# Kernel tuning notes

Hardware: AMD Instinct MI355X
Metric: run time of the kernel (lower is better)

Reference implementation:

```python
import jax, jax.numpy as jnp
import numpy as np

NEG_SLOPE = 0.2
EPS = 1e-16


def gat_layer(x, edge_index, edge_attr, W, We, a_src, a_dst, a_edge, bias,
              add_self_loops):
    """PyG GATConv with concat=True.
    x: [N, F_in], edge_index: [2, E] (row 0 = src j, row 1 = dst i),
    edge_attr: [E, De], W: [F_in, H*C], We: [De, H*C],
    a_src/a_dst/a_edge: [H, C], bias: [H*C].
    """
    N = x.shape[0]
    H, C = a_src.shape
    if add_self_loops:
        # fill_value='mean': self-loop edge_attr = mean of incoming edge_attr per node
        dst0 = edge_index[1]
        s = jax.ops.segment_sum(edge_attr, dst0, num_segments=N)
        cnt = jax.ops.segment_sum(jnp.ones((edge_attr.shape[0], 1), edge_attr.dtype),
                                  dst0, num_segments=N)
        loop_attr = s / jnp.maximum(cnt, 1.0)
        loop_idx = jnp.arange(N, dtype=edge_index.dtype)
        edge_index = jnp.concatenate(
            [edge_index, jnp.stack([loop_idx, loop_idx])], axis=1)
        edge_attr = jnp.concatenate([edge_attr, loop_attr], axis=0)

    src, dst = edge_index[0], edge_index[1]
    h = (x @ W).reshape(N, H, C)                       # [N, H, C]
    e = (edge_attr @ We).reshape(-1, H, C)             # [E, H, C]

    alpha_src = jnp.einsum('nhc,hc->nh', h, a_src)     # [N, H]
    alpha_dst = jnp.einsum('nhc,hc->nh', h, a_dst)     # [N, H]
    alpha_edge = jnp.einsum('ehc,hc->eh', e, a_edge)   # [E, H]

    alpha = alpha_src[src] + alpha_dst[dst] + alpha_edge
    alpha = jax.nn.leaky_relu(alpha, NEG_SLOPE)

    # segment softmax over destination node
    amax = jax.ops.segment_max(alpha, dst, num_segments=N)      # [N, H]
    ex = jnp.exp(alpha - amax[dst])
    denom = jax.ops.segment_sum(ex, dst, num_segments=N)        # [N, H]
    attn = ex / (denom[dst] + EPS)                               # [E, H]

    msg = h[src] * attn[:, :, None]                              # [E, H, C]
    out = jax.ops.segment_sum(msg, dst, num_segments=N)          # [N, H, C]
    return out.reshape(N, H * C) + bias


def setup_inputs() -> dict:
    key = jax.random.key(0)
    ks = jax.random.split(key, 16)
    N, E, F_in, C, H, De = 10000, 160000, 128, 64, 8, 1
    d1 = H * C  # 512

    def glorot(k, shape):
        fan = shape[0] + shape[-1]
        s = jnp.sqrt(6.0 / fan)
        return jax.random.uniform(k, shape, jnp.float32, -s, s)

    return {
        'x': jax.random.normal(ks[0], (N, F_in), jnp.float32),
        'edge_index': jax.random.randint(ks[1], (2, E), 0, N, jnp.int32),
        'edge_attr': jax.random.normal(ks[2], (E, De), jnp.float32),
        # layer 1 params
        'W1': glorot(ks[3], (F_in, d1)),
        'We1': glorot(ks[4], (De, d1)),
        'as1': glorot(ks[5], (H, C)),
        'ad1': glorot(ks[6], (H, C)),
        'ae1': glorot(ks[7], (H, C)),
        'b1': jnp.zeros((d1,), jnp.float32),
        # layer 2 params
        'W2': glorot(ks[8], (d1, d1)),
        'We2': glorot(ks[9], (De, d1)),
        'as2': glorot(ks[10], (H, C)),
        'ad2': glorot(ks[11], (H, C)),
        'ae2': glorot(ks[12], (H, C)),
        'b2': jnp.zeros((d1,), jnp.float32),
    }


def reference(x, edge_index, edge_attr,
              W1, We1, as1, ad1, ae1, b1,
              W2, We2, as2, ad2, ae2, b2):
    h = gat_layer(x, edge_index, edge_attr, W1, We1, as1, ad1, ae1, b1,
                  add_self_loops=False)
    h = jax.nn.relu(h)
    h = gat_layer(h, edge_index, edge_attr, W2, We2, as2, ad2, ae2, b2,
                  add_self_loops=True)
    return jnp.mean(h, axis=0)  # [512]
```

## Files before the change

### kernel.cpp

```cpp
#include <hip/hip_runtime.h>
#include <hip/hip_bf16.h>

#define HD __device__ __forceinline__
typedef unsigned short u16;
typedef __attribute__((ext_vector_type(8))) short bf16x8;
typedef __attribute__((ext_vector_type(4))) float f32x4;

HD u16 f2b(float f){
  unsigned u = __float_as_uint(f);
  unsigned r = (u + 0x7fffu + ((u>>16)&1u)) >> 16;
  return (u16)r;
}
HD float b2f(short s){ return __uint_as_float(((unsigned)(u16)s)<<16); }

__global__ void k_count(const int* __restrict__ dst, const float* __restrict__ ea,
                        int* cnt, float* easum, int E){
  int e = blockIdx.x*blockDim.x + threadIdx.x;
  if (e>=E) return;
  int d = dst[e];
  atomicAdd(&cnt[d],1);
  atomicAdd(&easum[d], ea[e]);
}

__global__ __launch_bounds__(1024) void k_scan(const int* __restrict__ cnt, int* offs, int N){
  __shared__ int lds[1024];
  const int chunk = (N + 1023)/1024;
  const int b = threadIdx.x*chunk;
  int s = 0;
  for (int i=0;i<chunk;++i){ int idx=b+i; if (idx<N) s += cnt[idx]; }
  lds[threadIdx.x] = s;
  __syncthreads();
  #pragma unroll
  for (int off=1; off<1024; off<<=1){
    int t = (threadIdx.x>=(unsigned)off)? lds[threadIdx.x-off] : 0;
    __syncthreads();
    lds[threadIdx.x] += t;
    __syncthreads();
  }
  int excl = lds[threadIdx.x] - s;
  for (int i=0;i<chunk;++i){
    int idx=b+i;
    if (idx<N){ offs[idx] = excl; excl += cnt[idx]; }
  }
  if (threadIdx.x==1023) offs[N] = lds[1023];
}

__global__ void k_scatter(const int* __restrict__ src, const int* __restrict__ dst,
                          const float* __restrict__ ea, const int* __restrict__ offs,
                          int* fill, int* srcs, float* eas, int E){
  int e = blockIdx.x*blockDim.x + threadIdx.x;
  if (e>=E) return;
  int d = dst[e];
  int p = offs[d] + atomicAdd(&fill[d],1);
  srcs[p] = src[e];
  eas[p]  = ea[e];
}

__global__ void k_loopattr(const int* __restrict__ cnt, const float* __restrict__ easum,
                           float* la, int N){
  int n = blockIdx.x*blockDim.x + threadIdx.x;
  if (n>=N) return;
  la[n] = easum[n] / fmaxf((float)cnt[n], 1.f);
}

__global__ __launch_bounds__(512) void k_wedot(const float* __restrict__ We1, const float* __restrict__ ae1,
                        const float* __restrict__ We2, const float* __restrict__ ae2,
                        float* wedot){
  int which = blockIdx.x;
  const float* We = which? We2 : We1;
  const float* ae = which? ae2 : ae1;
  int hh = threadIdx.x>>6, lane = threadIdx.x&63;
  float p = We[hh*64+lane]*ae[hh*64+lane];
  #pragma unroll
  for (int o=32;o;o>>=1) p += __shfl_down(p,o);
  if (lane==0) wedot[which*8+hh] = p;
}

__global__ void k_cast_bf16(const float* __restrict__ in, u16* __restrict__ out, int total4){
  int i = (blockIdx.x*blockDim.x + threadIdx.x);
  if (i>=total4) return;
  float4 v = *(const float4*)(in + (size_t)i*4);
  ushort4 o; o.x=f2b(v.x); o.y=f2b(v.y); o.z=f2b(v.z); o.w=f2b(v.w);
  *(ushort4*)(out + (size_t)i*4) = o;
}

__global__ __launch_bounds__(256) void k_transpose_cast(const float* __restrict__ W,
                                                        u16* __restrict__ Wt, int K, int N){
  __shared__ float T[64][65];
  int k0 = blockIdx.y*64, n0 = blockIdx.x*64;
  #pragma unroll
  for (int i=0;i<16;++i){
    int id = i*256 + threadIdx.x;
    int r = id>>6, c = id&63;
    T[r][c] = W[(size_t)(k0+r)*N + n0 + c];
  }
  __syncthreads();
  #pragma unroll
  for (int i=0;i<16;++i){
    int id = i*256 + threadIdx.x;
    int rr = id>>6, cc = id&63;
    Wt[(size_t)(n0+rr)*K + k0 + cc] = f2b(T[cc][rr]);
  }
}

__global__ __launch_bounds__(256) void k_gemm_mfma(
    const u16* __restrict__ A, const u16* __restrict__ Bt,
    u16* __restrict__ Cb, int M, int N, int K){
  __shared__ char lds[(128+64)*80];
  char* As = lds;
  char* Bs = lds + 128*80;
  const int tid = threadIdx.x;
  const int lane = tid & 63, w = tid >> 6;
  const int wr = w >> 1, wc = w & 1;
  const int l15 = lane & 15, l4 = lane >> 4;
  const int m0 = blockIdx.y*128, n0 = blockIdx.x*64;

  f32x4 acc[4][2] = {};
  int aoff[4], boff[2];
  #pragma unroll
  for (int i=0;i<4;++i) aoff[i] = (wr*64 + i*16 + l15)*80 + l4*16;
  #pragma unroll
  for (int j=0;j<2;++j) boff[j] = (wc*32 + j*16 + l15)*80 + l4*16;

  for (int k0=0; k0<K; k0+=32){
    #pragma unroll
    for (int i=0;i<2;++i){
      int cid = tid*2+i;
      int r = cid>>2, c = cid&3;
      int row = m0 + r;
      float4 v = make_float4(0.f,0.f,0.f,0.f);
      if (row < M) v = *(const float4*)(A + (size_t)row*K + k0 + c*8);
      *(float4*)(As + r*80 + c*16) = v;
    }
    {
      int r = tid>>2, c = tid&3;
      float4 v = *(const float4*)(Bt + (size_t)(n0+r)*K + k0 + c*8);
      *(float4*)(Bs + r*80 + c*16) = v;
    }
    __syncthreads();
    bf16x8 a[4], b[2];
    #pragma unroll
    for (int i=0;i<4;++i) a[i] = *reinterpret_cast<const bf16x8*>(As + aoff[i]);
    #pragma unroll
    for (int j=0;j<2;++j) b[j] = *reinterpret_cast<const bf16x8*>(Bs + boff[j]);
    #pragma unroll
    for (int i=0;i<4;++i)
      #pragma unroll
      for (int j=0;j<2;++j)
        acc[i][j] = __builtin_amdgcn_mfma_f32_16x16x32_bf16(a[i], b[j], acc[i][j], 0,0,0);
    __syncthreads();
  }
  #pragma unroll
  for (int i=0;i<4;++i){
    #pragma unroll
    for (int j=0;j<2;++j){
      #pragma unroll
      for (int r=0;r<4;++r){
        int row = m0 + wr*64 + i*16 + l4*4 + r;
        int col = n0 + wc*32 + j*16 + l15;
        if (row < M) Cb[(size_t)row*N + col] = f2b(acc[i][j][r]);
      }
    }
  }
}

__global__ __launch_bounds__(256) void k_alpha_nodes(const u16* __restrict__ hb,
    const float* __restrict__ a_s, const float* __restrict__ a_d,
    float* asrc, float* adst, int N){
  int n = blockIdx.x*4 + (threadIdx.x>>6);
  if (n>=N) return;
  int lane = threadIdx.x&63;
  int c0 = lane*8;
  bf16x8 v = *(const bf16x8*)(hb + (size_t)n*512 + c0);
  float s = 0.f, d = 0.f;
  #pragma unroll
  for (int j=0;j<8;++j){
    float f = b2f(v[j]);
    s = fmaf(f, a_s[c0+j], s);
    d = fmaf(f, a_d[c0+j], d);
  }
  #pragma unroll
  for (int o=1;o<8;o<<=1){ s += __shfl_xor(s,o); d += __shfl_xor(d,o); }
  if ((lane&7)==0){ int hh = lane>>3; asrc[n*8+hh]=s; adst[n*8+hh]=d; }
}

__global__ __launch_bounds__(256) void k_softmax(
    const int* __restrict__ srcs, const float* __restrict__ eas,
    const int* __restrict__ offs,
    const float* __restrict__ asrc, const float* __restrict__ adst,
    const float* __restrict__ wedot, const float* __restrict__ la,
    float* __restrict__ exn, float* __restrict__ inv, float* __restrict__ aselfx,
    int N, int self_flag){
  int n = blockIdx.x*4 + (threadIdx.x>>6);
  if (n>=N) return;
  int lane = threadIdx.x&63;
  int hh = lane&7, esub = lane>>3;
  int beg = offs[n], end = offs[n+1];
  float wd = wedot[hh];
  float adn = adst[n*8+hh];

  float mx = -1e30f;
  for (int p0=beg; p0<end; p0+=8){
    int p = p0 + esub;
    if (p<end){
      int s = srcs[p];
      float a = asrc[s*8+hh] + adn + eas[p]*wd;
      a = a>0.f ? a : 0.2f*a;
      exn[(size_t)p*8+hh] = a;
      mx = fmaxf(mx, a);
    }
  }
  float aself = 0.f;
  if (self_flag){
    float a = asrc[n*8+hh] + adn + la[n]*wd;
    aself = a>0.f ? a : 0.2f*a;
    if (esub==0) mx = fmaxf(mx, aself);
  }
  mx = fmaxf(mx, __shfl_xor(mx, 8));
  mx = fmaxf(mx, __shfl_xor(mx, 16));
  mx = fmaxf(mx, __shfl_xor(mx, 32));

  float sum = 0.f;
  for (int p0=beg; p0<end; p0+=8){
    int p = p0 + esub;
    if (p<end){
      float x = __expf(exn[(size_t)p*8+hh] - mx);
      exn[(size_t)p*8+hh] = x;
      sum += x;
    }
  }
  float xs = 0.f;
  if (self_flag && esub==0){ xs = __expf(aself - mx); sum += xs; }
  sum += __shfl_xor(sum, 8);
  sum += __shfl_xor(sum, 16);
  sum += __shfl_xor(sum, 32);
  if (esub==0){
    inv[n*8+hh] = 1.f/(sum + 1e-16f);
    if (self_flag) aselfx[n*8+hh] = xs;
  }
}

__global__ __launch_bounds__(256) void k_aggregate(const u16* __restrict__ hb,
    const float* __restrict__ exn, const int* __restrict__ srcs,
    const int* __restrict__ offs, const float* __restrict__ bias,
    const float* __restrict__ inv, const float* __restrict__ aselfx,
    float* __restrict__ outf, u16* __restrict__ outb,
    int N, int relu_flag, int self_flag){
  int n = blockIdx.x*4 + (threadIdx.x>>6);
  if (n>=N) return;
  int lane = threadIdx.x&63;
  int hh = lane>>3;
  int c0 = lane*8;
  int beg = offs[n], end = offs[n+1];
  float acc[8] = {};
  int p = beg;
  for (; p+2<=end; p+=2){
    int s0 = srcs[p], s1 = srcs[p+1];
    float e0 = exn[(size_t)p*8 + hh];
    float e1 = exn[(size_t)(p+1)*8 + hh];
    bf16x8 v0 = *(const bf16x8*)(hb + (size_t)s0*512 + c0);
    bf16x8 v1 = *(const bf16x8*)(hb + (size_t)s1*512 + c0);
    #pragma unroll
    for (int j=0;j<8;++j)
      acc[j] = fmaf(e0, b2f(v0[j]), fmaf(e1, b2f(v1[j]), acc[j]));
  }
  if (p<end){
    int s0 = srcs[p];
    float e0 = exn[(size_t)p*8 + hh];
    bf16x8 v0 = *(const bf16x8*)(hb + (size_t)s0*512 + c0);
    #pragma unroll
    for (int j=0;j<8;++j) acc[j] = fmaf(e0, b2f(v0[j]), acc[j]);
  }
  if (self_flag){
    float es = aselfx[n*8+hh];
    bf16x8 v = *(const bf16x8*)(hb + (size_t)n*512 + c0);
    #pragma unroll
    for (int j=0;j<8;++j) acc[j] = fmaf(es, b2f(v[j]), acc[j]);
  }
  float iv = inv[n*8+hh];
  float val[8];
  #pragma unroll
  for (int j=0;j<8;++j){
    val[j] = acc[j]*iv + bias[c0+j];
    if (relu_flag) val[j] = fmaxf(val[j], 0.f);
  }
  if (outb){
    bf16x8 ov;
    #pragma unroll
    for (int j=0;j<8;++j) ov[j] = (short)f2b(val[j]);
    *(bf16x8*)(outb + (size_t)n*512 + c0) = ov;
  } else {
    *(float4*)(outf + (size_t)n*512 + c0)     = make_float4(val[0],val[1],val[2],val[3]);
    *(float4*)(outf + (size_t)n*512 + c0 + 4) = make_float4(val[4],val[5],val[6],val[7]);
  }
}

__global__ __launch_bounds__(512) void k_colmean(const float* __restrict__ out2, float* __restrict__ o,
                          int N, float invN){
  int c = threadIdx.x;
  int n0 = blockIdx.x*16;
  int nend = min(n0+16, N);
  float s = 0.f;
  for (int n=n0;n<nend;++n) s += out2[(size_t)n*512 + c];
  atomicAdd(&o[c], s*invN);
}

extern "C" void kernel_launch(void* const* d_in, const int* in_sizes, int n_in,
                              void* d_out, int out_size, void* d_ws, size_t ws_size,
                              hipStream_t stream){
  const float* x   = (const float*)d_in[0];
  const int* eidx  = (const int*)d_in[1];
  const float* ea  = (const float*)d_in[2];
  const float* W1  = (const float*)d_in[3];
  const float* We1 = (const float*)d_in[4];
  const float* as1 = (const float*)d_in[5];
  const float* ad1 = (const float*)d_in[6];
  const float* ae1 = (const float*)d_in[7];
  const float* b1  = (const float*)d_in[8];
  const float* W2  = (const float*)d_in[9];
  const float* We2 = (const float*)d_in[10];
  const float* as2 = (const float*)d_in[11];
  const float* ad2 = (const float*)d_in[12];
  const float* ae2 = (const float*)d_in[13];
  const float* b2  = (const float*)d_in[14];
  float* outp = (float*)d_out;

  const int FIN = 128, D1 = 512;
  const int N = in_sizes[0]/FIN;
  const int E = in_sizes[1]/2;
  const int* srcA = eidx;
  const int* dstA = eidx + E;

  char* ws = (char*)d_ws;
  size_t o = 0;
  auto alloc = [&](size_t bytes)->void*{
    void* p = ws + o; o = (o + bytes + 255) & ~(size_t)255; return p;
  };
  u16*   hb1   = (u16*)  alloc((size_t)N*D1*2);
  u16*   hb2   = (u16*)  alloc((size_t)N*D1*2);
  u16*   out1rb= (u16*)  alloc((size_t)N*D1*2);
  float* out2  = (float*)alloc((size_t)N*D1*4);
  u16*   xb    = (u16*)  alloc((size_t)N*FIN*2);
  u16*   W1t   = (u16*)  alloc((size_t)D1*FIN*2);
  u16*   W2t   = (u16*)  alloc((size_t)D1*D1*2);
  float* exn   = (float*)alloc((size_t)E*8*4);
  int*   srcs  = (int*)  alloc((size_t)E*4);
  float* eas   = (float*)alloc((size_t)E*4);
  int*   offs  = (int*)  alloc((size_t)(N+1)*4);
  size_t zbeg = o;
  int*   cnt   = (int*)  alloc((size_t)N*4);
  int*   fill  = (int*)  alloc((size_t)N*4);
  float* easum = (float*)alloc((size_t)N*4);
  size_t zend = o;
  float* asrc  = (float*)alloc((size_t)N*8*4);
  float* adst  = (float*)alloc((size_t)N*8*4);
  float* la    = (float*)alloc((size_t)N*4);
  float* inv   = (float*)alloc((size_t)N*8*4);
  float* aselfx= (float*)alloc((size_t)N*8*4);
  float* wedot = (float*)alloc(64);
  (void)ws_size; (void)n_in;

  hipMemsetAsync(ws + zbeg, 0, zend - zbeg, stream);
  hipMemsetAsync(d_out, 0, (size_t)out_size*sizeof(float), stream);

  dim3 b256(256);
  int ge = (E+255)/256;
  int gn4 = (N+3)/4;

  k_count   <<<ge, b256, 0, stream>>>(dstA, ea, cnt, easum, E);
  k_scan    <<<1, 1024, 0, stream>>>(cnt, offs, N);
  k_scatter <<<ge, b256, 0, stream>>>(srcA, dstA, ea, offs, fill, srcs, eas, E);
  k_loopattr<<<(N+255)/256, b256, 0, stream>>>(cnt, easum, la, N);
  k_wedot   <<<2, 512, 0, stream>>>(We1, ae1, We2, ae2, wedot);
  k_cast_bf16<<<((N*FIN/4)+255)/256, b256, 0, stream>>>(x, xb, N*FIN/4);
  k_transpose_cast<<<dim3(D1/64, FIN/64), b256, 0, stream>>>(W1, W1t, FIN, D1);
  k_transpose_cast<<<dim3(D1/64, D1/64),  b256, 0, stream>>>(W2, W2t, D1, D1);

  k_gemm_mfma<<<dim3(D1/64, (N+127)/128), b256, 0, stream>>>(xb, W1t, hb1, N, D1, FIN);
  k_alpha_nodes<<<gn4, b256, 0, stream>>>(hb1, as1, ad1, asrc, adst, N);
  k_softmax<<<gn4, b256, 0, stream>>>(srcs, eas, offs, asrc, adst, wedot, la,
                                      exn, inv, aselfx, N, 0);
  k_aggregate<<<gn4, b256, 0, stream>>>(hb1, exn, srcs, offs, b1, inv,
                                        (const float*)nullptr, (float*)nullptr,
                                        out1rb, N, 1, 0);

  k_gemm_mfma<<<dim3(D1/64, (N+127)/128), b256, 0, stream>>>(out1rb, W2t, hb2, N, D1, D1);
  k_alpha_nodes<<<gn4, b256, 0, stream>>>(hb2, as2, ad2, asrc, adst, N);
  k_softmax<<<gn4, b256, 0, stream>>>(srcs, eas, offs, asrc, adst, wedot+8, la,
                                      exn, inv, aselfx, N, 1);
  k_aggregate<<<gn4, b256, 0, stream>>>(hb2, exn, srcs, offs, b2, inv,
                                        aselfx, out2, (u16*)nullptr, N, 0, 1);

  k_colmean<<<(N+15)/16, 512, 0, stream>>>(out2, outp, N, 1.0f/(float)N);
}
```

Measured before the change: 195.0 us.

## Fuse softmax with aggregation, merge prep kernels, widen GEMM tile, bf16 layer-2 output

Merges the per-node softmax and aggregation kernels into one, so normalizers stay in registers and each wave reads back its own exp values right after writing them. The small prep kernels are combined into two launches. The MFMA GEMM tile widens from 128x64 to 128x128 for more B reuse. The layer-2 output is stored as bf16 before the column mean, which halves that traffic but adds rounding error.

```diff
diff --git a/kernel.cpp b/kernel.cpp
--- a/kernel.cpp
+++ b/kernel.cpp
@@ -56,17 +56,18 @@
   eas[p]  = ea[e];
 }
 
-__global__ void k_loopattr(const int* __restrict__ cnt, const float* __restrict__ easum,
-                           float* la, int N){
-  int n = blockIdx.x*blockDim.x + threadIdx.x;
-  if (n>=N) return;
-  la[n] = easum[n] / fmaxf((float)cnt[n], 1.f);
-}
-
-__global__ __launch_bounds__(512) void k_wedot(const float* __restrict__ We1, const float* __restrict__ ae1,
-                        const float* __restrict__ We2, const float* __restrict__ ae2,
-                        float* wedot){
-  int which = blockIdx.x;
+__global__ __launch_bounds__(512) void k_prep_small(
+    const int* __restrict__ cnt, const float* __restrict__ easum, float* la, int N,
+    const float* __restrict__ We1, const float* __restrict__ ae1,
+    const float* __restrict__ We2, const float* __restrict__ ae2,
+    float* wedot, int nbLoop){
+  int bx = blockIdx.x;
+  if (bx < nbLoop){
+    int n = bx*512 + threadIdx.x;
+    if (n<N) la[n] = easum[n] / fmaxf((float)cnt[n], 1.f);
+    return;
+  }
+  int which = bx - nbLoop;
   const float* We = which? We2 : We1;
   const float* ae = which? ae2 : ae1;
   int hh = threadIdx.x>>6, lane = threadIdx.x&63;
@@ -76,23 +77,32 @@
   if (lane==0) wedot[which*8+hh] = p;
 }
 
-__global__ void k_cast_bf16(const float* __restrict__ in, u16* __restrict__ out, int total4){
-  int i = (blockIdx.x*blockDim.x + threadIdx.x);
-  if (i>=total4) return;
-  float4 v = *(const float4*)(in + (size_t)i*4);
-  ushort4 o; o.x=f2b(v.x); o.y=f2b(v.y); o.z=f2b(v.z); o.w=f2b(v.w);
-  *(ushort4*)(out + (size_t)i*4) = o;
-}
-
-__global__ __launch_bounds__(256) void k_transpose_cast(const float* __restrict__ W,
-                                                        u16* __restrict__ Wt, int K, int N){
+__global__ __launch_bounds__(256) void k_prep_cast(
+    const float* __restrict__ x, u16* __restrict__ xb, int total4,
+    const float* __restrict__ W1, u16* __restrict__ W1t,
+    const float* __restrict__ W2, u16* __restrict__ W2t,
+    int nbCast, int nbW1){
   __shared__ float T[64][65];
-  int k0 = blockIdx.y*64, n0 = blockIdx.x*64;
+  int bx = blockIdx.x;
+  if (bx < nbCast){
+    int i = bx*256 + threadIdx.x;
+    if (i<total4){
+      float4 v = *(const float4*)(x + (size_t)i*4);
+      ushort4 o; o.x=f2b(v.x); o.y=f2b(v.y); o.z=f2b(v.z); o.w=f2b(v.w);
+      *(ushort4*)(xb + (size_t)i*4) = o;
+    }
+    return;
+  }
+  const float* W; u16* Wt; int K, Nn, t;
+  if (bx < nbCast + nbW1){ t = bx - nbCast;        W = W1; Wt = W1t; K = 128; Nn = 512; }
+  else                   { t = bx - nbCast - nbW1; W = W2; Wt = W2t; K = 512; Nn = 512; }
+  int nt = Nn/64;
+  int k0 = (t/nt)*64, n0 = (t%nt)*64;
   #pragma unroll
   for (int i=0;i<16;++i){
     int id = i*256 + threadIdx.x;
     int r = id>>6, c = id&63;
-    T[r][c] = W[(size_t)(k0+r)*N + n0 + c];
+    T[r][c] = W[(size_t)(k0+r)*Nn + n0 + c];
   }
   __syncthreads();
   #pragma unroll
@@ -106,21 +116,21 @@
 __global__ __launch_bounds__(256) void k_gemm_mfma(
     const u16* __restrict__ A, const u16* __restrict__ Bt,
     u16* __restrict__ Cb, int M, int N, int K){
-  __shared__ char lds[(128+64)*80];
+  __shared__ char lds[256*80];
   char* As = lds;
   char* Bs = lds + 128*80;
   const int tid = threadIdx.x;
   const int lane = tid & 63, w = tid >> 6;
   const int wr = w >> 1, wc = w & 1;
   const int l15 = lane & 15, l4 = lane >> 4;
-  const int m0 = blockIdx.y*128, n0 = blockIdx.x*64;
-
-  f32x4 acc[4][2] = {};
-  int aoff[4], boff[2];
+  const int m0 = blockIdx.y*128, n0 = blockIdx.x*128;
+
+  f32x4 acc[4][4] = {};
+  int aoff[4], boff[4];
   #pragma unroll
   for (int i=0;i<4;++i) aoff[i] = (wr*64 + i*16 + l15)*80 + l4*16;
   #pragma unroll
-  for (int j=0;j<2;++j) boff[j] = (wc*32 + j*16 + l15)*80 + l4*16;
+  for (int j=0;j<4;++j) boff[j] = (wc*64 + j*16 + l15)*80 + l4*16;
 
   for (int k0=0; k0<K; k0+=32){
     #pragma unroll
@@ -132,32 +142,34 @@
       if (row < M) v = *(const float4*)(A + (size_t)row*K + k0 + c*8);
       *(float4*)(As + r*80 + c*16) = v;
     }
-    {
-      int r = tid>>2, c = tid&3;
+    #pragma unroll
+    for (int i=0;i<2;++i){
+      int cid = tid*2+i;
+      int r = cid>>2, c = cid&3;
       float4 v = *(const float4*)(Bt + (size_t)(n0+r)*K + k0 + c*8);
       *(float4*)(Bs + r*80 + c*16) = v;
     }
     __syncthreads();
-    bf16x8 a[4], b[2];
+    bf16x8 a[4], b[4];
     #pragma unroll
     for (int i=0;i<4;++i) a[i] = *reinterpret_cast<const bf16x8*>(As + aoff[i]);
     #pragma unroll
-    for (int j=0;j<2;++j) b[j] = *reinterpret_cast<const bf16x8*>(Bs + boff[j]);
+    for (int j=0;j<4;++j) b[j] = *reinterpret_cast<const bf16x8*>(Bs + boff[j]);
     #pragma unroll
     for (int i=0;i<4;++i)
       #pragma unroll
-      for (int j=0;j<2;++j)
+      for (int j=0;j<4;++j)
         acc[i][j] = __builtin_amdgcn_mfma_f32_16x16x32_bf16(a[i], b[j], acc[i][j], 0,0,0);
     __syncthreads();
   }
   #pragma unroll
   for (int i=0;i<4;++i){
     #pragma unroll
-    for (int j=0;j<2;++j){
+    for (int j=0;j<4;++j){
       #pragma unroll
       for (int r=0;r<4;++r){
         int row = m0 + wr*64 + i*16 + l4*4 + r;
-        int col = n0 + wc*32 + j*16 + l15;
+        int col = n0 + wc*64 + j*16 + l15;
         if (row < M) Cb[(size_t)row*N + col] = f2b(acc[i][j][r]);
       }
     }
@@ -184,13 +196,14 @@
   if ((lane&7)==0){ int hh = lane>>3; asrc[n*8+hh]=s; adst[n*8+hh]=d; }
 }
 
-__global__ __launch_bounds__(256) void k_softmax(
+__global__ __launch_bounds__(256) void k_softagg(const u16* __restrict__ hb,
     const int* __restrict__ srcs, const float* __restrict__ eas,
     const int* __restrict__ offs,
     const float* __restrict__ asrc, const float* __restrict__ adst,
     const float* __restrict__ wedot, const float* __restrict__ la,
-    float* __restrict__ exn, float* __restrict__ inv, float* __restrict__ aselfx,
-    int N, int self_flag){
+    const float* __restrict__ bias, float* __restrict__ exn,
+    u16* __restrict__ outb,
+    int N, int relu_flag, int self_flag){
   int n = blockIdx.x*4 + (threadIdx.x>>6);
   if (n>=N) return;
   int lane = threadIdx.x&63;
@@ -210,11 +223,11 @@
       mx = fmaxf(mx, a);
     }
   }
-  float aself = 0.f;
+  float aselfa = 0.f;
   if (self_flag){
     float a = asrc[n*8+hh] + adn + la[n]*wd;
-    aself = a>0.f ? a : 0.2f*a;
-    if (esub==0) mx = fmaxf(mx, aself);
+    aselfa = a>0.f ? a : 0.2f*a;
+    mx = fmaxf(mx, aselfa);
   }
   mx = fmaxf(mx, __shfl_xor(mx, 8));
   mx = fmaxf(mx, __shfl_xor(mx, 16));
@@ -229,35 +242,25 @@
       sum += x;
     }
   }
-  float xs = 0.f;
-  if (self_flag && esub==0){ xs = __expf(aself - mx); sum += xs; }
+  float xs = self_flag ? __expf(aselfa - mx) : 0.f;
+  if (esub==0) sum += xs;
   sum += __shfl_xor(sum, 8);
   sum += __shfl_xor(sum, 16);
   sum += __shfl_xor(sum, 32);
-  if (esub==0){
-    inv[n*8+hh] = 1.f/(sum + 1e-16f);
-    if (self_flag) aselfx[n*8+hh] = xs;
-  }
-}
-
-__global__ __launch_bounds__(256) void k_aggregate(const u16* __restrict__ hb,
-    const float* __restrict__ exn, const int* __restrict__ srcs,
-    const int* __restrict__ offs, const float* __restrict__ bias,
-    const float* __restrict__ inv, const float* __restrict__ aselfx,
-    float* __restrict__ outf, u16* __restrict__ outb,
-    int N, int relu_flag, int self_flag){
-  int n = blockIdx.x*4 + (threadIdx.x>>6);
-  if (n>=N) return;
-  int lane = threadIdx.x&63;
-  int hh = lane>>3;
+  float invv = 1.f/(sum + 1e-16f);
+
+  __threadfence();
+
+  int ahh = lane>>3;
+  float iv = __shfl(invv, ahh);
+  float es = __shfl(xs,   ahh);
   int c0 = lane*8;
-  int beg = offs[n], end = offs[n+1];
   float acc[8] = {};
   int p = beg;
   for (; p+2<=end; p+=2){
     int s0 = srcs[p], s1 = srcs[p+1];
-    float e0 = exn[(size_t)p*8 + hh];
-    float e1 = exn[(size_t)(p+1)*8 + hh];
+    float e0 = exn[(size_t)p*8 + ahh];
+    float e1 = exn[(size_t)(p+1)*8 + ahh];
     bf16x8 v0 = *(const bf16x8*)(hb + (size_t)s0*512 + c0);
     bf16x8 v1 = *(const bf16x8*)(hb + (size_t)s1*512 + c0);
     #pragma unroll
@@ -266,42 +269,33 @@
   }
   if (p<end){
     int s0 = srcs[p];
-    float e0 = exn[(size_t)p*8 + hh];
+    float e0 = exn[(size_t)p*8 + ahh];
     bf16x8 v0 = *(const bf16x8*)(hb + (size_t)s0*512 + c0);
     #pragma unroll
     for (int j=0;j<8;++j) acc[j] = fmaf(e0, b2f(v0[j]), acc[j]);
   }
   if (self_flag){
-    float es = aselfx[n*8+hh];
     bf16x8 v = *(const bf16x8*)(hb + (size_t)n*512 + c0);
     #pragma unroll
     for (int j=0;j<8;++j) acc[j] = fmaf(es, b2f(v[j]), acc[j]);
   }
-  float iv = inv[n*8+hh];
-  float val[8];
+  bf16x8 ov;
   #pragma unroll
   for (int j=0;j<8;++j){
-    val[j] = acc[j]*iv + bias[c0+j];
-    if (relu_flag) val[j] = fmaxf(val[j], 0.f);
-  }
-  if (outb){
-    bf16x8 ov;
-    #pragma unroll
-    for (int j=0;j<8;++j) ov[j] = (short)f2b(val[j]);
-    *(bf16x8*)(outb + (size_t)n*512 + c0) = ov;
-  } else {
-    *(float4*)(outf + (size_t)n*512 + c0)     = make_float4(val[0],val[1],val[2],val[3]);
-    *(float4*)(outf + (size_t)n*512 + c0 + 4) = make_float4(val[4],val[5],val[6],val[7]);
-  }
-}
-
-__global__ __launch_bounds__(512) void k_colmean(const float* __restrict__ out2, float* __restrict__ o,
-                          int N, float invN){
+    float val = acc[j]*iv + bias[c0+j];
+    if (relu_flag) val = fmaxf(val, 0.f);
+    ov[j] = (short)f2b(val);
+  }
+  *(bf16x8*)(outb + (size_t)n*512 + c0) = ov;
+}
+
+__global__ __launch_bounds__(512) void k_colmean(const u16* __restrict__ out2b,
+                          float* __restrict__ o, int N, float invN){
   int c = threadIdx.x;
   int n0 = blockIdx.x*16;
   int nend = min(n0+16, N);
   float s = 0.f;
-  for (int n=n0;n<nend;++n) s += out2[(size_t)n*512 + c];
+  for (int n=n0;n<nend;++n) s += b2f(out2b[(size_t)n*512 + c]);
   atomicAdd(&o[c], s*invN);
 }
 
@@ -339,7 +333,7 @@
   u16*   hb1   = (u16*)  alloc((size_t)N*D1*2);
   u16*   hb2   = (u16*)  alloc((size_t)N*D1*2);
   u16*   out1rb= (u16*)  alloc((size_t)N*D1*2);
-  float* out2  = (float*)alloc((size_t)N*D1*4);
+  u16*   out2b = (u16*)  alloc((size_t)N*D1*2);
   u16*   xb    = (u16*)  alloc((size_t)N*FIN*2);
   u16*   W1t   = (u16*)  alloc((size_t)D1*FIN*2);
   u16*   W2t   = (u16*)  alloc((size_t)D1*D1*2);
@@ -355,8 +349,6 @@
   float* asrc  = (float*)alloc((size_t)N*8*4);
   float* adst  = (float*)alloc((size_t)N*8*4);
   float* la    = (float*)alloc((size_t)N*4);
-  float* inv   = (float*)alloc((size_t)N*8*4);
-  float* aselfx= (float*)alloc((size_t)N*8*4);
   float* wedot = (float*)alloc(64);
   (void)ws_size; (void)n_in;
 
@@ -370,26 +362,27 @@
   k_count   <<<ge, b256, 0, stream>>>(dstA, ea, cnt, easum, E);
   k_scan    <<<1, 1024, 0, stream>>>(cnt, offs, N);
   k_scatter <<<ge, b256, 0, stream>>>(srcA, dstA, ea, offs, fill, srcs, eas, E);
-  k_loopattr<<<(N+255)/256, b256, 0, stream>>>(cnt, easum, la, N);
-  k_wedot   <<<2, 512, 0, stream>>>(We1, ae1, We2, ae2, wedot);
-  k_cast_bf16<<<((N*FIN/4)+255)/256, b256, 0, stream>>>(x, xb, N*FIN/4);
-  k_transpose_cast<<<dim3(D1/64, FIN/64), b256, 0, stream>>>(W1, W1t, FIN, D1);
-  k_transpose_cast<<<dim3(D1/64, D1/64),  b256, 0, stream>>>(W2, W2t, D1, D1);
-
-  k_gemm_mfma<<<dim3(D1/64, (N+127)/128), b256, 0, stream>>>(xb, W1t, hb1, N, D1, FIN);
+  {
+    int nbLoop = (N+511)/512;
+    k_prep_small<<<nbLoop+2, 512, 0, stream>>>(cnt, easum, la, N,
+                                               We1, ae1, We2, ae2, wedot, nbLoop);
+    int total4 = N*FIN/4;
+    int nbCast = (total4+255)/256;
+    int nbW1 = (FIN/64)*(D1/64);
+    int nbW2 = (D1/64)*(D1/64);
+    k_prep_cast<<<nbCast+nbW1+nbW2, b256, 0, stream>>>(x, xb, total4,
+                                                       W1, W1t, W2, W2t, nbCast, nbW1);
+  }
+
+  k_gemm_mfma<<<dim3(D1/128, (N+127)/128), b256, 0, stream>>>(xb, W1t, hb1, N, D1, FIN);
   k_alpha_nodes<<<gn4, b256, 0, stream>>>(hb1, as1, ad1, asrc, adst, N);
-  k_softmax<<<gn4, b256, 0, stream>>>(srcs, eas, offs, asrc, adst, wedot, la,
-                                      exn, inv, aselfx, N, 0);
-  k_aggregate<<<gn4, b256, 0, stream>>>(hb1, exn, srcs, offs, b1, inv,
-                                        (const float*)nullptr, (float*)nullptr,
-                                        out1rb, N, 1, 0);
-
-  k_gemm_mfma<<<dim3(D1/64, (N+127)/128), b256, 0, stream>>>(out1rb, W2t, hb2, N, D1, D1);
+  k_softagg<<<gn4, b256, 0, stream>>>(hb1, srcs, eas, offs, asrc, adst, wedot, la,
+                                      b1, exn, out1rb, N, 1, 0);
+
+  k_gemm_mfma<<<dim3(D1/128, (N+127)/128), b256, 0, stream>>>(out1rb, W2t, hb2, N, D1, D1);
   k_alpha_nodes<<<gn4, b256, 0, stream>>>(hb2, as2, ad2, asrc, adst, N);
-  k_softmax<<<gn4, b256, 0, stream>>>(srcs, eas, offs, asrc, adst, wedot+8, la,
-                                      exn, inv, aselfx, N, 1);
-  k_aggregate<<<gn4, b256, 0, stream>>>(hb2, exn, srcs, offs, b2, inv,
-                                        aselfx, out2, (u16*)nullptr, N, 0, 1);
-
-  k_colmean<<<(N+15)/16, 512, 0, stream>>>(out2, outp, N, 1.0f/(float)N);
-}
+  k_softagg<<<gn4, b256, 0, stream>>>(hb2, srcs, eas, offs, asrc, adst, wedot+8, la,
+                                      b2, exn, out2b, N, 0, 1);
+
+  k_colmean<<<(N+15)/16, 512, 0, stream>>>(out2b, outp, N, 1.0f/(float)N);
+}
```

Measured after the change: 663.2 us. 3.4x slower.
